# Performance work log

Measured on AMD Instinct MI355X. Metric: run time of the kernel, lower is better.

The kernel has to match this reference:

```python
import math
import jax, jax.numpy as jnp
import numpy as np

CLUSTER_RATIO1 = 0.0625
CLUSTER_RATIO2 = 0.35
K_LAYER1 = 8
K_LAYER2 = 3


def _dpc_knn(x, cluster_num, k, key):
    """Density-peak clustering with KNN density. x: [B,N,C] -> idx_cluster [B,N]."""
    B, N, C = x.shape
    sq = jnp.sum(x * x, axis=-1)  # [B,N]
    d2 = sq[:, :, None] + sq[:, None, :] - 2.0 * jnp.einsum('bnc,bmc->bnm', x, x)
    dist = jnp.sqrt(jnp.maximum(d2, 0.0)) / jnp.sqrt(jnp.asarray(C, x.dtype))  # cdist / C**0.5
    # k nearest (smallest) distances
    neg_dn, _ = jax.lax.top_k(-dist, k)
    dist_nearest = -neg_dn  # [B,N,k]
    density = jnp.exp(-jnp.mean(dist_nearest ** 2, axis=-1))
    density = density + jax.random.uniform(key, density.shape, dtype=density.dtype) * 1e-6
    mask = (density[:, None, :] > density[:, :, None]).astype(x.dtype)  # [B,N,N]
    dist_max = jnp.max(dist.reshape(B, -1), axis=-1)[:, None, None]
    parent_dist = jnp.min(dist * mask + dist_max * (1.0 - mask), axis=-1)  # [B,N]
    score = parent_dist * density
    _, index_down = jax.lax.top_k(score, cluster_num)  # [B,cluster_num] cluster centers
    # assign each token to nearest center
    dm = jnp.take_along_axis(dist, index_down[:, :, None], axis=1)  # [B,cluster_num,N]
    idx_cluster = jnp.argmin(dm, axis=1)  # [B,N]
    bidx = jnp.arange(B)[:, None]
    idx_cluster = idx_cluster.at[bidx, index_down].set(
        jnp.broadcast_to(jnp.arange(cluster_num)[None, :], index_down.shape))
    return idx_cluster


def _merge_tokens(x, idx_cluster, cluster_num):
    """Weighted (uniform) scatter-mean of tokens into clusters. x: [B,N,C]."""
    B, N, C = x.shape
    flat = (idx_cluster + jnp.arange(B)[:, None] * cluster_num).reshape(-1)  # [B*N]
    ones = jnp.ones((B * N,), x.dtype)
    all_w = jax.ops.segment_sum(ones, flat, num_segments=B * cluster_num) + 1e-6
    norm_w = 1.0 / all_w[flat]  # token_weight == 1
    merged = jax.ops.segment_sum(x.reshape(B * N, C) * norm_w[:, None], flat,
                                 num_segments=B * cluster_num)
    return merged.reshape(B, cluster_num, C)


def _group(meta1, meta2, idx_cluster2, score_w, score_b):
    """Reorder [meta2[v]; members of cluster v from meta1] per cluster, scaled by modulation."""
    T, K1, C = meta1.shape
    K2 = meta2.shape[1]
    modu = jax.nn.softmax(meta2.mean(axis=2) @ score_w.T + score_b, axis=-1)  # [T,K2]
    # composite sort key: (cluster_id, 0 for meta2 center, 1+i for meta1 member i) -> stable grouping
    cid = jnp.concatenate([jnp.broadcast_to(jnp.arange(K2)[None, :], (T, K2)),
                           idx_cluster2], axis=1)  # [T,K2+K1]
    pos = jnp.concatenate([jnp.zeros((T, K2), jnp.int32),
                           jnp.broadcast_to(jnp.arange(1, K1 + 1, dtype=jnp.int32)[None, :], (T, K1))],
                          axis=1)
    sort_key = cid * (K1 + 2) + pos
    order = jnp.argsort(sort_key, axis=1)  # stable; keys are unique anyway
    tokens = jnp.concatenate([meta2, meta1], axis=1)  # [T,K2+K1,C]
    sorted_tokens = jnp.take_along_axis(tokens, order[:, :, None], axis=1)
    sorted_cid = jnp.take_along_axis(cid, order, axis=1)
    scale = jnp.take_along_axis(modu, sorted_cid, axis=1)  # [T,K2+K1]
    return sorted_tokens * scale[:, :, None]


def setup_inputs() -> dict:
    key = jax.random.key(0)
    k1, k2, k3 = jax.random.split(key, 3)
    T, N, C = 128, 256, 1408
    vis_embed = jax.random.normal(k1, (T, N, C), dtype=jnp.float32)
    score_w = jax.random.normal(k2, (6, 6), dtype=jnp.float32) * 0.1
    score_b = jax.random.normal(k3, (6,), dtype=jnp.float32) * 0.1
    return {"vis_embed": vis_embed, "score_w": score_w, "score_b": score_b}


def reference(vis_embed, score_w, score_b):
    T, N, C = vis_embed.shape
    cn1 = max(math.ceil(N * CLUSTER_RATIO1), 1)      # 16
    cn2 = max(math.ceil(cn1 * CLUSTER_RATIO2), 1)    # 6
    nk = jax.random.split(jax.random.key(42), 2)
    idx1 = _dpc_knn(vis_embed, cn1, K_LAYER1, nk[0])
    meta1 = _merge_tokens(vis_embed, idx1, cn1)       # [T,16,C]
    idx2 = _dpc_knn(meta1, cn2, K_LAYER2, nk[1])
    meta2 = _merge_tokens(meta1, idx2, cn2)           # [T,6,C]
    return _group(meta1, meta2, idx2, score_w, score_b)  # [T,22,C]
```

## Files before the change

kernel.cpp:

```cpp
#include <hip/hip_runtime.h>
#include <math.h>

#define T_BATCH 128
#define N_TOK   256
#define C_DIM   1408
#define CN1     16
#define KNN1    8
#define CN2     6
#define KNN2    3
#define NOUT    22
#define LS2     36

typedef __attribute__((ext_vector_type(4))) short sh4;
typedef __attribute__((ext_vector_type(8))) short sh8;
typedef __attribute__((ext_vector_type(4))) float f32x4;

union frag_u { sh4 h[2]; sh8 v; };

__device__ inline sh8 ld_frag(const short* p) {
    frag_u u;
    u.h[0] = *(const sh4*)p;
    u.h[1] = *(const sh4*)(p + 4);
    return u.v;
}

__device__ inline void split2(float v0, float v1, unsigned& hip, unsigned& lop) {
    unsigned u0 = __float_as_uint(v0);
    unsigned u1 = __float_as_uint(v1);
    hip = (u0 >> 16) | (u1 & 0xFFFF0000u);
    float l0 = v0 - __uint_as_float(u0 & 0xFFFF0000u);
    float l1 = v1 - __uint_as_float(u1 & 0xFFFF0000u);
    unsigned w0 = __float_as_uint(l0);
    unsigned w1 = __float_as_uint(l1);
    w0 = w0 + 0x7FFFu + ((w0 >> 16) & 1u);
    w1 = w1 + 0x7FFFu + ((w1 >> 16) & 1u);
    lop = (w0 >> 16) | (w1 & 0xFFFF0000u);
}

#define INS8(m, v) {                                   \
    float _x = (v);                                    \
    _Pragma("unroll")                                  \
    for (int _q = 0; _q < 8; _q++) {                   \
        float _lo = fminf(m[_q], _x);                  \
        _x = fmaxf(m[_q], _x);                         \
        m[_q] = _lo;                                   \
    }                                                  \
}

__global__ __launch_bounds__(512, 2) void gemm_dist_half(const float* __restrict__ x,
                                                         float* __restrict__ dist) {
    const int id = blockIdx.x;
    const int r  = id & 7;
    const int u  = id >> 3;
    const int h  = u & 1;
    const int t  = (u >> 1) * 8 + r;
    const float* X = x + (size_t)t * N_TOK * C_DIM;

    __shared__ short Phi[N_TOK * LS2];
    __shared__ short Plo[N_TOK * LS2];
    __shared__ float nred[512];
    __shared__ float sn[N_TOK];

    const int tid  = threadIdx.x;
    const int wave = tid >> 6;
    const int lane = tid & 63;
    const int wr   = wave >> 2;
    const int wc   = wave & 3;
    const int srow = tid >> 1;
    const int sq   = tid & 1;
    const int fr   = lane & 15;
    const int fq   = lane >> 4;

    f32x4 acc[4][4];
#pragma unroll
    for (int a = 0; a < 4; a++)
#pragma unroll
        for (int b = 0; b < 4; b++) acc[a][b] = (f32x4){0.f, 0.f, 0.f, 0.f};

    const float* Row = X + (size_t)srow * C_DIM + sq * 16;
    float nA = 0.f;

    float4 a0 = *(const float4*)(Row + 0);
    float4 a1 = *(const float4*)(Row + 4);
    float4 a2 = *(const float4*)(Row + 8);
    float4 a3 = *(const float4*)(Row + 12);

    for (int k0 = 0; k0 < C_DIM; k0 += 32) {
        float av[16];
        av[0]  = a0.x; av[1]  = a0.y; av[2]  = a0.z; av[3]  = a0.w;
        av[4]  = a1.x; av[5]  = a1.y; av[6]  = a1.z; av[7]  = a1.w;
        av[8]  = a2.x; av[9]  = a2.y; av[10] = a2.z; av[11] = a2.w;
        av[12] = a3.x; av[13] = a3.y; av[14] = a3.z; av[15] = a3.w;
#pragma unroll
        for (int e = 0; e < 16; e++) nA += av[e] * av[e];
        unsigned hh[8], ll[8];
#pragma unroll
        for (int q = 0; q < 8; q++) split2(av[2 * q], av[2 * q + 1], hh[q], ll[q]);

        __syncthreads();
        {
            uint2* WH = (uint2*)&Phi[srow * LS2 + sq * 16];
            uint2* WL = (uint2*)&Plo[srow * LS2 + sq * 16];
#pragma unroll
            for (int q = 0; q < 4; q++) {
                uint2 vh; vh.x = hh[2 * q]; vh.y = hh[2 * q + 1];
                uint2 vl; vl.x = ll[2 * q]; vl.y = ll[2 * q + 1];
                WH[q] = vh;
                WL[q] = vl;
            }
        }
        __syncthreads();

        const int k1 = k0 + 32;
        if (k1 < C_DIM) {
            a0 = *(const float4*)(Row + k1);
            a1 = *(const float4*)(Row + k1 + 4);
            a2 = *(const float4*)(Row + k1 + 8);
            a3 = *(const float4*)(Row + k1 + 12);
        }

        sh8 fAh[4], fAl[4];
#pragma unroll
        for (int mt = 0; mt < 4; mt++) {
            int ao = (h * 128 + wr * 64 + mt * 16 + fr) * LS2 + fq * 8;
            fAh[mt] = ld_frag(&Phi[ao]);
            fAl[mt] = ld_frag(&Plo[ao]);
        }
#pragma unroll
        for (int nt = 0; nt < 4; nt++) {
            int bo = (wc * 64 + nt * 16 + fr) * LS2 + fq * 8;
            sh8 fBh = ld_frag(&Phi[bo]);
            sh8 fBl = ld_frag(&Plo[bo]);
#pragma unroll
            for (int mt = 0; mt < 4; mt++) {
                acc[mt][nt] = __builtin_amdgcn_mfma_f32_16x16x32_bf16(fAh[mt], fBh, acc[mt][nt], 0, 0, 0);
                acc[mt][nt] = __builtin_amdgcn_mfma_f32_16x16x32_bf16(fAh[mt], fBl, acc[mt][nt], 0, 0, 0);
                acc[mt][nt] = __builtin_amdgcn_mfma_f32_16x16x32_bf16(fAl[mt], fBh, acc[mt][nt], 0, 0, 0);
            }
        }
    }

    nred[tid] = nA;
    __syncthreads();
    if (tid < N_TOK) sn[tid] = nred[2 * tid] + nred[2 * tid + 1];
    __syncthreads();

    const float inv_sqrtC = 1.0f / sqrtf((float)C_DIM);
    float* Dt = dist + (size_t)t * N_TOK * N_TOK;
#pragma unroll
    for (int mt = 0; mt < 4; mt++)
#pragma unroll
        for (int nt = 0; nt < 4; nt++) {
            int jg = wc * 64 + nt * 16 + fr;
            float sqj = sn[jg];
            int i0 = h * 128 + wr * 64 + mt * 16 + fq * 4;
#pragma unroll
            for (int rr = 0; rr < 4; rr++) {
                int ig = i0 + rr;
                float d2 = sn[ig] + sqj - 2.0f * acc[mt][nt][rr];
                float v = (ig == jg) ? 0.0f : sqrtf(fmaxf(d2, 0.0f)) * inv_sqrtC;
                Dt[(size_t)ig * N_TOK + jg] = v;
            }
        }
}

__global__ __launch_bounds__(1024) void dpc1_fused(const float* __restrict__ dist,
                                                   int* __restrict__ memb,
                                                   int* __restrict__ cntg,
                                                   int* __restrict__ offg) {
    const int t    = blockIdx.x;
    const int tid  = threadIdx.x;
    const int col  = tid & 255;
    const int h    = tid >> 8;
    const int lane = tid & 63;
    const int wid  = tid >> 6;
    const float* D = dist + (size_t)t * N_TOK * N_TOK;

    __shared__ float dens_s[N_TOK];
    __shared__ float lists[KNN1][1024];
    __shared__ float red[1024];
    __shared__ float rmax16[16];
    __shared__ unsigned long long wred[16];
    __shared__ int centers[CN1];
    __shared__ int bks[N_TOK];
    __shared__ int cnt_s[CN1], off_s[CN1];

    float c0[8], c1[8];
#pragma unroll
    for (int q = 0; q < 8; q++) { c0[q] = 3.4e38f; c1[q] = 3.4e38f; }
    float mx = 0.f;
    const float* base = D + (size_t)(h * 64) * N_TOK + col;
    for (int jj = 0; jj < 64; jj += 2) {
        float d0 = base[(size_t)(jj + 0) * N_TOK];
        float d1 = base[(size_t)(jj + 1) * N_TOK];
        mx = fmaxf(mx, fmaxf(d0, d1));
        INS8(c0, d0); INS8(c1, d1);
    }
#pragma unroll
    for (int q = 0; q < 8; q++) { INS8(c0, c1[q]); }
#pragma unroll
    for (int q = 0; q < 8; q++) lists[q][tid] = c0[q];
#pragma unroll
    for (int off = 32; off > 0; off >>= 1) mx = fmaxf(mx, __shfl_xor(mx, off));
    if (lane == 0) rmax16[wid] = mx;
    __syncthreads();
    float dmax = rmax16[0];
#pragma unroll
    for (int w = 1; w < 16; w++) dmax = fmaxf(dmax, rmax16[w]);

    if (h == 0) {
#pragma unroll
        for (int s = 1; s < 4; s++)
#pragma unroll
            for (int q = 0; q < 8; q++) { float v = lists[q][col + s * 256]; INS8(c0, v); }
        float s2 = 0.f;
#pragma unroll
        for (int q = 0; q < 8; q++) s2 += c0[q] * c0[q];
        dens_s[col] = expf(-s2 / (float)KNN1);
    }
    __syncthreads();
    const float dens = dens_s[col];

    float p0 = dmax, p1 = dmax;
    const float* dsh = dens_s + h * 64;
    for (int jj = 0; jj < 64; jj += 2) {
        float d0 = base[(size_t)(jj + 0) * N_TOK];
        float d1 = base[(size_t)(jj + 1) * N_TOK];
        p0 = (dsh[jj + 0] > dens) ? fminf(p0, d0) : p0;
        p1 = (dsh[jj + 1] > dens) ? fminf(p1, d1) : p1;
    }
    red[tid] = fminf(p0, p1);
    __syncthreads();
    float score = 0.f;
    if (h == 0)
        score = fminf(fminf(red[col], red[col + 256]),
                      fminf(red[col + 512], red[col + 768])) * dens;

    unsigned long long key = 0;
    if (h == 0)
        key = ((unsigned long long)__float_as_uint(score) << 32) | (unsigned)(65535 - col);
    for (int k = 0; k < CN1; k++) {
        unsigned long long mm = key;
#pragma unroll
        for (int off = 32; off > 0; off >>= 1) {
            unsigned long long o = __shfl_xor(mm, off);
            mm = (o > mm) ? o : mm;
        }
        if (lane == 0) wred[wid] = mm;
        __syncthreads();
        unsigned long long b = wred[0];
#pragma unroll
        for (int w = 1; w < 16; w++) b = (wred[w] > b) ? wred[w] : b;
        int idx = 65535 - (int)(b & 0xFFFFull);
        if (tid == 0) centers[k] = idx;
        if (tid == idx) key = 0;
        __syncthreads();
    }

    int bk = 0;
    if (h == 0) {
        float bd = 3.4e38f;
#pragma unroll
        for (int k = 0; k < CN1; k++) {
            float d = D[(size_t)centers[k] * N_TOK + col];
            if (d < bd) { bd = d; bk = k; }
        }
#pragma unroll
        for (int k = 0; k < CN1; k++) if (col == centers[k]) bk = k;
        bks[col] = bk;
    }
    __syncthreads();
    if (tid < CN1) {
        int c = 0;
        for (int j = 0; j < N_TOK; j++) c += (bks[j] == tid);
        cnt_s[tid] = c;
    }
    __syncthreads();
    if (tid == 0) {
        int o = 0;
        for (int q = 0; q < CN1; q++) { off_s[q] = o; o += cnt_s[q]; }
    }
    __syncthreads();
    if (h == 0) {
        int rank = 0;
        for (int j = 0; j < col; j++) rank += (bks[j] == bk);
        memb[t * N_TOK + off_s[bk] + rank] = col;
    }
    if (tid < CN1) {
        cntg[t * CN1 + tid] = cnt_s[tid];
        offg[t * CN1 + tid] = off_s[tid];
    }
}

__global__ __launch_bounds__(256) void merge1_kernel(const float* __restrict__ x,
                                                     const int* __restrict__ memb,
                                                     const int* __restrict__ cntg,
                                                     const int* __restrict__ offg,
                                                     float* __restrict__ meta1) {
    const int q   = blockIdx.x;
    const int t   = blockIdx.y;
    const int tid = threadIdx.x;
    const int n    = cntg[t * CN1 + q];
    const int base = t * N_TOK + offg[t * CN1 + q];
    const int c0 = tid, c1 = tid + 256;
    const bool act1 = (c1 < C_DIM / 4);
    const float4* xb = (const float4*)(x + (size_t)t * N_TOK * C_DIM);
    const int stride4 = C_DIM / 4;

    float4 s0 = {0.f, 0.f, 0.f, 0.f};
    float4 s1 = {0.f, 0.f, 0.f, 0.f};
    int m = 0;
    for (; m + 4 <= n; m += 4) {
        int r0 = memb[base + m + 0];
        int r1 = memb[base + m + 1];
        int r2 = memb[base + m + 2];
        int r3 = memb[base + m + 3];
        float4 a0 = xb[(size_t)r0 * stride4 + c0];
        float4 a1 = xb[(size_t)r1 * stride4 + c0];
        float4 a2 = xb[(size_t)r2 * stride4 + c0];
        float4 a3 = xb[(size_t)r3 * stride4 + c0];
        s0.x += a0.x; s0.y += a0.y; s0.z += a0.z; s0.w += a0.w;
        s0.x += a1.x; s0.y += a1.y; s0.z += a1.z; s0.w += a1.w;
        s0.x += a2.x; s0.y += a2.y; s0.z += a2.z; s0.w += a2.w;
        s0.x += a3.x; s0.y += a3.y; s0.z += a3.z; s0.w += a3.w;
        if (act1) {
            float4 b0 = xb[(size_t)r0 * stride4 + c1];
            float4 b1 = xb[(size_t)r1 * stride4 + c1];
            float4 b2 = xb[(size_t)r2 * stride4 + c1];
            float4 b3 = xb[(size_t)r3 * stride4 + c1];
            s1.x += b0.x; s1.y += b0.y; s1.z += b0.z; s1.w += b0.w;
            s1.x += b1.x; s1.y += b1.y; s1.z += b1.z; s1.w += b1.w;
            s1.x += b2.x; s1.y += b2.y; s1.z += b2.z; s1.w += b2.w;
            s1.x += b3.x; s1.y += b3.y; s1.z += b3.z; s1.w += b3.w;
        }
    }
    for (; m < n; m++) {
        int r0 = memb[base + m];
        float4 a0 = xb[(size_t)r0 * stride4 + c0];
        s0.x += a0.x; s0.y += a0.y; s0.z += a0.z; s0.w += a0.w;
        if (act1) {
            float4 b0 = xb[(size_t)r0 * stride4 + c1];
            s1.x += b0.x; s1.y += b0.y; s1.z += b0.z; s1.w += b0.w;
        }
    }
    float w = 1.0f / ((float)n + 1e-6f);
    float4* mr = (float4*)(meta1 + ((size_t)t * CN1 + q) * C_DIM);
    float4 o0; o0.x = s0.x * w; o0.y = s0.y * w; o0.z = s0.z * w; o0.w = s0.w * w;
    mr[c0] = o0;
    if (act1) {
        float4 o1; o1.x = s1.x * w; o1.y = s1.y * w; o1.z = s1.z * w; o1.w = s1.w * w;
        mr[c1] = o1;
    }
}

__global__ __launch_bounds__(1024) void layer2_kernel(const float* __restrict__ meta1,
                                                      const float* __restrict__ score_w,
                                                      const float* __restrict__ score_b,
                                                      float* __restrict__ out) {
    const int t   = blockIdx.x;
    const int tid = threadIdx.x;
    const float* M = meta1 + (size_t)t * CN1 * C_DIM;

    __shared__ float buf[CN1][132];
    __shared__ float d2s[CN1][CN1];
    __shared__ float m2[CN2][C_DIM];
    __shared__ float dens[CN1], scor[CN1], nrm[CN1], rmx[CN1];
    __shared__ int   centers[CN2], idx2s[CN1], cnt2[CN2];
    __shared__ float modu[CN2], msum[CN2];
    __shared__ int   srcRow[NOUT], cidArr[NOUT];
    __shared__ float dmax_sh;

    const int ti = (tid < 256) ? (tid >> 4) : 0;
    const int tj = tid & 15;

    float acc = 0.f;
    for (int c0 = 0; c0 < C_DIM; c0 += 128) {
        for (int e = tid; e < CN1 * 128; e += 1024) {
            int r = e >> 7, c = e & 127;
            buf[r][c] = M[(size_t)r * C_DIM + c0 + c];
        }
        __syncthreads();
        if (tid < 256) {
#pragma unroll
            for (int cc = 0; cc < 128; cc += 4) {
                float4 a = *(const float4*)&buf[ti][cc];
                float4 b = *(const float4*)&buf[tj][cc];
                acc += a.x * b.x + a.y * b.y + a.z * b.z + a.w * b.w;
            }
        }
        __syncthreads();
    }
    if (tid < 256 && ti == tj) nrm[ti] = acc;
    __syncthreads();

    const float inv_sqrtC = 1.0f / sqrtf((float)C_DIM);
    if (tid < 256) {
        float d2 = nrm[ti] + nrm[tj] - 2.f * acc;
        d2s[ti][tj] = sqrtf(fmaxf(d2, 0.f)) * inv_sqrtC;
    }
    __syncthreads();

    if (tid < CN1) {
        float m0 = 3.4e38f, m1 = 3.4e38f, m2v = 3.4e38f, mx = 0.f;
        for (int j = 0; j < CN1; j++) {
            float d = d2s[tid][j];
            mx = fmaxf(mx, d);
            if (d < m2v) {
                m2v = d;
                if (m2v < m1) { float tmp = m2v; m2v = m1; m1 = tmp; }
                if (m1 < m0)  { float tmp = m1;  m1 = m0;  m0 = tmp; }
            }
        }
        dens[tid] = expf(-(m0 * m0 + m1 * m1 + m2v * m2v) / (float)KNN2);
        rmx[tid] = mx;
    }
    __syncthreads();
    if (tid == 0) {
        float g = 0.f;
        for (int j = 0; j < CN1; j++) g = fmaxf(g, rmx[j]);
        dmax_sh = g;
    }
    __syncthreads();

    if (tid < CN1) {
        float di = dens[tid];
        float pd = dmax_sh;
        for (int j = 0; j < CN1; j++)
            if (dens[j] > di) pd = fminf(pd, d2s[tid][j]);
        scor[tid] = pd * di;
    }
    __syncthreads();

    if (tid == 0) {
        for (int k = 0; k < CN2; k++) {
            float best = -3.4e38f; int bi = 0;
            for (int j = 0; j < CN1; j++)
                if (scor[j] > best) { best = scor[j]; bi = j; }
            centers[k] = bi;
            scor[bi] = -3.4e38f;
        }
    }
    __syncthreads();

    if (tid < CN1) {
        float bd = 3.4e38f; int bk = 0;
#pragma unroll
        for (int k = 0; k < CN2; k++) {
            float d = d2s[centers[k]][tid];
            if (d < bd) { bd = d; bk = k; }
        }
#pragma unroll
        for (int k = 0; k < CN2; k++) if (tid == centers[k]) bk = k;
        idx2s[tid] = bk;
    }
    __syncthreads();

    if (tid == 0) {
        for (int v = 0; v < CN2; v++) cnt2[v] = 0;
        for (int i = 0; i < CN1; i++) cnt2[idx2s[i]]++;
        int slot = 0;
        for (int v = 0; v < CN2; v++) {
            srcRow[slot] = CN1 + v; cidArr[slot] = v; slot++;
            for (int i = 0; i < CN1; i++)
                if (idx2s[i] == v) { srcRow[slot] = i; cidArr[slot] = v; slot++; }
        }
        for (int v = 0; v < CN2; v++) msum[v] = 0.f;
    }
    __syncthreads();

    float ls[CN2] = {0.f, 0.f, 0.f, 0.f, 0.f, 0.f};
    for (int ch = tid; ch < C_DIM; ch += 1024) {
        float a6[CN2] = {0.f, 0.f, 0.f, 0.f, 0.f, 0.f};
        for (int r = 0; r < CN1; r++) {
            float v = M[(size_t)r * C_DIM + ch];
            int c = idx2s[r];
#pragma unroll
            for (int q = 0; q < CN2; q++) a6[q] += (c == q) ? v : 0.f;
        }
#pragma unroll
        for (int q = 0; q < CN2; q++) {
            float mv = a6[q] / ((float)cnt2[q] + 1e-6f);
            m2[q][ch] = mv;
            ls[q] += mv;
        }
    }
#pragma unroll
    for (int q = 0; q < CN2; q++) atomicAdd(&msum[q], ls[q]);
    __syncthreads();

    if (tid == 0) {
        float mean[CN2], lg[CN2];
        for (int v = 0; v < CN2; v++) mean[v] = msum[v] / (float)C_DIM;
        float mxl = -3.4e38f;
        for (int u = 0; u < CN2; u++) {
            float s = score_b[u];
            for (int v = 0; v < CN2; v++) s += mean[v] * score_w[u * CN2 + v];
            lg[u] = s;
            mxl = fmaxf(mxl, s);
        }
        float den = 0.f;
        for (int u = 0; u < CN2; u++) { lg[u] = expf(lg[u] - mxl); den += lg[u]; }
        for (int u = 0; u < CN2; u++) modu[u] = lg[u] / den;
    }
    __syncthreads();

    float* ob = out + (size_t)t * NOUT * C_DIM;
    for (int ch = tid; ch < C_DIM; ch += 1024) {
#pragma unroll
        for (int s = 0; s < NOUT; s++) {
            int r = srcRow[s];
            float v = (r < CN1) ? M[(size_t)r * C_DIM + ch] : m2[r - CN1][ch];
            ob[(size_t)s * C_DIM + ch] = v * modu[cidArr[s]];
        }
    }
}

extern "C" void kernel_launch(void* const* d_in, const int* in_sizes, int n_in,
                              void* d_out, int out_size, void* d_ws, size_t ws_size,
                              hipStream_t stream) {
    const float* x  = (const float*)d_in[0];
    const float* sw = (const float*)d_in[1];
    const float* sb = (const float*)d_in[2];
    float* out = (float*)d_out;

    float* ws     = (float*)d_ws;
    float* dist   = ws;
    float* meta1  = dist + (size_t)T_BATCH * N_TOK * N_TOK;
    int*   memb   = (int*)(meta1 + (size_t)T_BATCH * CN1 * C_DIM);
    int*   cntg   = memb + (size_t)T_BATCH * N_TOK;
    int*   offg   = cntg + T_BATCH * CN1;

    gemm_dist_half<<<256, 512, 0, stream>>>(x, dist);
    dpc1_fused<<<T_BATCH, 1024, 0, stream>>>(dist, memb, cntg, offg);
    merge1_kernel<<<dim3(CN1, T_BATCH), 256, 0, stream>>>(x, memb, cntg, offg, meta1);
    layer2_kernel<<<T_BATCH, 1024, 0, stream>>>(meta1, sw, sb, out);
}
```

Measured before the change: 435.1 us.

## Double-buffer LDS tiles in distance GEMM and switch hi/lo split to fp16

The distance GEMM now keeps two LDS buffers for the split-precision tiles, so the next k-slice is loaded and converted while MFMAs run on the current one. This drops one barrier per iteration. The hi/lo split moves from a bit-masked bf16 split to an fp16 split built with packed conversion instructions and f16 MFMAs, which should cost fewer ALU operations to produce. Global loads are remapped so that 8 threads cover a row with float4 loads across 4 row groups, which changes coalescing and the squared-norm reduction. The risks are fp16 range limits on large input values and double the LDS use, which could lower occupancy.

Result: slower. 449.8 us (+3.4%).

```diff
diff --git a/kernel.cpp b/kernel.cpp
--- a/kernel.cpp
+++ b/kernel.cpp
@@ -10,12 +10,17 @@
 #define KNN2    3
 #define NOUT    22
 #define LS2     36
+#define NKS     44
 
 typedef __attribute__((ext_vector_type(4))) short sh4;
 typedef __attribute__((ext_vector_type(8))) short sh8;
 typedef __attribute__((ext_vector_type(4))) float f32x4;
+typedef __fp16 h2v __attribute__((ext_vector_type(2)));
+typedef __fp16 h8v __attribute__((ext_vector_type(8)));
 
 union frag_u { sh4 h[2]; sh8 v; };
+union h8u { sh8 s; h8v h; };
+union h2u { h2v h; unsigned u; };
 
 __device__ inline sh8 ld_frag(const short* p) {
     frag_u u;
@@ -24,17 +29,10 @@
     return u.v;
 }
 
-__device__ inline void split2(float v0, float v1, unsigned& hip, unsigned& lop) {
-    unsigned u0 = __float_as_uint(v0);
-    unsigned u1 = __float_as_uint(v1);
-    hip = (u0 >> 16) | (u1 & 0xFFFF0000u);
-    float l0 = v0 - __uint_as_float(u0 & 0xFFFF0000u);
-    float l1 = v1 - __uint_as_float(u1 & 0xFFFF0000u);
-    unsigned w0 = __float_as_uint(l0);
-    unsigned w1 = __float_as_uint(l1);
-    w0 = w0 + 0x7FFFu + ((w0 >> 16) & 1u);
-    w1 = w1 + 0x7FFFu + ((w1 >> 16) & 1u);
-    lop = (w0 >> 16) | (w1 & 0xFFFF0000u);
+__device__ inline h8v ld_frag_h(const short* p) {
+    h8u u;
+    u.s = ld_frag(p);
+    return u.h;
 }
 
 #define INS8(m, v) {                                   \
@@ -47,8 +45,8 @@
     }                                                  \
 }
 
-__global__ __launch_bounds__(512, 2) void gemm_dist_half(const float* __restrict__ x,
-                                                         float* __restrict__ dist) {
+__global__ __launch_bounds__(512, 2) void gemm_dist_f16(const float* __restrict__ x,
+                                                        float* __restrict__ dist) {
     const int id = blockIdx.x;
     const int r  = id & 7;
     const int u  = id >> 3;
@@ -56,9 +54,9 @@
     const int t  = (u >> 1) * 8 + r;
     const float* X = x + (size_t)t * N_TOK * C_DIM;
 
-    __shared__ short Phi[N_TOK * LS2];
-    __shared__ short Plo[N_TOK * LS2];
-    __shared__ float nred[512];
+    __shared__ short Phi[2][N_TOK * LS2];
+    __shared__ short Plo[2][N_TOK * LS2];
+    __shared__ float nred2[N_TOK][8];
     __shared__ float sn[N_TOK];
 
     const int tid  = threadIdx.x;
@@ -66,8 +64,8 @@
     const int lane = tid & 63;
     const int wr   = wave >> 2;
     const int wc   = wave & 3;
-    const int srow = tid >> 1;
-    const int sq   = tid & 1;
+    const int rr   = tid >> 3;
+    const int c8   = tid & 7;
     const int fr   = lane & 15;
     const int fq   = lane >> 4;
 
@@ -76,73 +74,102 @@
     for (int a = 0; a < 4; a++)
 #pragma unroll
         for (int b = 0; b < 4; b++) acc[a][b] = (f32x4){0.f, 0.f, 0.f, 0.f};
-
-    const float* Row = X + (size_t)srow * C_DIM + sq * 16;
-    float nA = 0.f;
-
-    float4 a0 = *(const float4*)(Row + 0);
-    float4 a1 = *(const float4*)(Row + 4);
-    float4 a2 = *(const float4*)(Row + 8);
-    float4 a3 = *(const float4*)(Row + 12);
-
-    for (int k0 = 0; k0 < C_DIM; k0 += 32) {
-        float av[16];
-        av[0]  = a0.x; av[1]  = a0.y; av[2]  = a0.z; av[3]  = a0.w;
-        av[4]  = a1.x; av[5]  = a1.y; av[6]  = a1.z; av[7]  = a1.w;
-        av[8]  = a2.x; av[9]  = a2.y; av[10] = a2.z; av[11] = a2.w;
-        av[12] = a3.x; av[13] = a3.y; av[14] = a3.z; av[15] = a3.w;
-#pragma unroll
-        for (int e = 0; e < 16; e++) nA += av[e] * av[e];
-        unsigned hh[8], ll[8];
-#pragma unroll
-        for (int q = 0; q < 8; q++) split2(av[2 * q], av[2 * q + 1], hh[q], ll[q]);
-
-        __syncthreads();
-        {
-            uint2* WH = (uint2*)&Phi[srow * LS2 + sq * 16];
-            uint2* WL = (uint2*)&Plo[srow * LS2 + sq * 16];
-#pragma unroll
-            for (int q = 0; q < 4; q++) {
-                uint2 vh; vh.x = hh[2 * q]; vh.y = hh[2 * q + 1];
-                uint2 vl; vl.x = ll[2 * q]; vl.y = ll[2 * q + 1];
-                WH[q] = vh;
-                WL[q] = vl;
-            }
-        }
-        __syncthreads();
-
-        const int k1 = k0 + 32;
-        if (k1 < C_DIM) {
-            a0 = *(const float4*)(Row + k1);
-            a1 = *(const float4*)(Row + k1 + 4);
-            a2 = *(const float4*)(Row + k1 + 8);
-            a3 = *(const float4*)(Row + k1 + 12);
-        }
-
-        sh8 fAh[4], fAl[4];
+    float nacc[4] = {0.f, 0.f, 0.f, 0.f};
+
+    const float* Rbase = X + (size_t)rr * C_DIM + c8 * 4;
+
+    float4 fb[4];
+#pragma unroll
+    for (int p = 0; p < 4; p++)
+        fb[p] = *(const float4*)(Rbase + (size_t)(64 * p) * C_DIM);
+#pragma unroll
+    for (int p = 0; p < 4; p++) {
+        const float4 f = fb[p];
+        nacc[p] += f.x * f.x + f.y * f.y + f.z * f.z + f.w * f.w;
+        h2v h0 = __builtin_amdgcn_cvt_pkrtz(f.x, f.y);
+        h2v h1 = __builtin_amdgcn_cvt_pkrtz(f.z, f.w);
+        float l0 = f.x - (float)h0[0];
+        float l1 = f.y - (float)h0[1];
+        float l2 = f.z - (float)h1[0];
+        float l3 = f.w - (float)h1[1];
+        h2v g0 = __builtin_amdgcn_cvt_pkrtz(l0, l1);
+        h2v g1 = __builtin_amdgcn_cvt_pkrtz(l2, l3);
+        h2u a0, a1, b0, b1;
+        a0.h = h0; a1.h = h1; b0.h = g0; b1.h = g1;
+        uint2 vh; vh.x = a0.u; vh.y = a1.u;
+        uint2 vl; vl.x = b0.u; vl.y = b1.u;
+        *(uint2*)&Phi[0][(64 * p + rr) * LS2 + c8 * 4] = vh;
+        *(uint2*)&Plo[0][(64 * p + rr) * LS2 + c8 * 4] = vl;
+    }
+    __syncthreads();
+
+    for (int ks = 0; ks < NKS; ks++) {
+        const int cur = ks & 1;
+        const int k1  = (ks + 1) * 32;
+        const bool more = (k1 < C_DIM);
+
+        if (more) {
+#pragma unroll
+            for (int p = 0; p < 4; p++)
+                fb[p] = *(const float4*)(Rbase + (size_t)(64 * p) * C_DIM + k1);
+        }
+
+        const short* PH = Phi[cur];
+        const short* PL = Plo[cur];
+        h8v fAh[4], fAl[4];
 #pragma unroll
         for (int mt = 0; mt < 4; mt++) {
             int ao = (h * 128 + wr * 64 + mt * 16 + fr) * LS2 + fq * 8;
-            fAh[mt] = ld_frag(&Phi[ao]);
-            fAl[mt] = ld_frag(&Plo[ao]);
+            fAh[mt] = ld_frag_h(&PH[ao]);
+            fAl[mt] = ld_frag_h(&PL[ao]);
         }
 #pragma unroll
         for (int nt = 0; nt < 4; nt++) {
             int bo = (wc * 64 + nt * 16 + fr) * LS2 + fq * 8;
-            sh8 fBh = ld_frag(&Phi[bo]);
-            sh8 fBl = ld_frag(&Plo[bo]);
+            h8v fBh = ld_frag_h(&PH[bo]);
+            h8v fBl = ld_frag_h(&PL[bo]);
 #pragma unroll
             for (int mt = 0; mt < 4; mt++) {
-                acc[mt][nt] = __builtin_amdgcn_mfma_f32_16x16x32_bf16(fAh[mt], fBh, acc[mt][nt], 0, 0, 0);
-                acc[mt][nt] = __builtin_amdgcn_mfma_f32_16x16x32_bf16(fAh[mt], fBl, acc[mt][nt], 0, 0, 0);
-                acc[mt][nt] = __builtin_amdgcn_mfma_f32_16x16x32_bf16(fAl[mt], fBh, acc[mt][nt], 0, 0, 0);
+                acc[mt][nt] = __builtin_amdgcn_mfma_f32_16x16x32_f16(fAh[mt], fBh, acc[mt][nt], 0, 0, 0);
+                acc[mt][nt] = __builtin_amdgcn_mfma_f32_16x16x32_f16(fAh[mt], fBl, acc[mt][nt], 0, 0, 0);
+                acc[mt][nt] = __builtin_amdgcn_mfma_f32_16x16x32_f16(fAl[mt], fBh, acc[mt][nt], 0, 0, 0);
             }
         }
-    }
-
-    nred[tid] = nA;
-    __syncthreads();
-    if (tid < N_TOK) sn[tid] = nred[2 * tid] + nred[2 * tid + 1];
+
+        if (more) {
+            const int nb = cur ^ 1;
+#pragma unroll
+            for (int p = 0; p < 4; p++) {
+                const float4 f = fb[p];
+                nacc[p] += f.x * f.x + f.y * f.y + f.z * f.z + f.w * f.w;
+                h2v h0 = __builtin_amdgcn_cvt_pkrtz(f.x, f.y);
+                h2v h1 = __builtin_amdgcn_cvt_pkrtz(f.z, f.w);
+                float l0 = f.x - (float)h0[0];
+                float l1 = f.y - (float)h0[1];
+                float l2 = f.z - (float)h1[0];
+                float l3 = f.w - (float)h1[1];
+                h2v g0 = __builtin_amdgcn_cvt_pkrtz(l0, l1);
+                h2v g1 = __builtin_amdgcn_cvt_pkrtz(l2, l3);
+                h2u a0, a1, b0, b1;
+                a0.h = h0; a1.h = h1; b0.h = g0; b1.h = g1;
+                uint2 vh; vh.x = a0.u; vh.y = a1.u;
+                uint2 vl; vl.x = b0.u; vl.y = b1.u;
+                *(uint2*)&Phi[nb][(64 * p + rr) * LS2 + c8 * 4] = vh;
+                *(uint2*)&Plo[nb][(64 * p + rr) * LS2 + c8 * 4] = vl;
+            }
+        }
+        __syncthreads();
+    }
+
+#pragma unroll
+    for (int p = 0; p < 4; p++) nred2[64 * p + rr][c8] = nacc[p];
+    __syncthreads();
+    if (tid < N_TOK) {
+        float s = 0.f;
+#pragma unroll
+        for (int c = 0; c < 8; c++) s += nred2[tid][c];
+        sn[tid] = s;
+    }
     __syncthreads();
 
     const float inv_sqrtC = 1.0f / sqrtf((float)C_DIM);
@@ -155,9 +182,9 @@
             float sqj = sn[jg];
             int i0 = h * 128 + wr * 64 + mt * 16 + fq * 4;
 #pragma unroll
-            for (int rr = 0; rr < 4; rr++) {
-                int ig = i0 + rr;
-                float d2 = sn[ig] + sqj - 2.0f * acc[mt][nt][rr];
+            for (int rr2 = 0; rr2 < 4; rr2++) {
+                int ig = i0 + rr2;
+                float d2 = sn[ig] + sqj - 2.0f * acc[mt][nt][rr2];
                 float v = (ig == jg) ? 0.0f : sqrtf(fmaxf(d2, 0.0f)) * inv_sqrtC;
                 Dt[(size_t)ig * N_TOK + jg] = v;
             }
@@ -530,7 +557,7 @@
     int*   cntg   = memb + (size_t)T_BATCH * N_TOK;
     int*   offg   = cntg + T_BATCH * CN1;
 
-    gemm_dist_half<<<256, 512, 0, stream>>>(x, dist);
+    gemm_dist_f16<<<256, 512, 0, stream>>>(x, dist);
     dpc1_fused<<<T_BATCH, 1024, 0, stream>>>(dist, memb, cntg, offg);
     merge1_kernel<<<dim3(CN1, T_BATCH), 256, 0, stream>>>(x, memb, cntg, offg, meta1);
     layer2_kernel<<<T_BATCH, 1024, 0, stream>>>(meta1, sw, sb, out);
```
